# Performance work log

Measured on AMD Instinct MI355X. Metric: run time of the kernel, lower is better.

## Reference

```python
import jax, jax.numpy as jnp
import numpy as np

N_NODES = 100000
N_EDGES = 1600000
N_GRAPHS = 2048
BN_EPS = 1e-5


def _bn(h, gamma, beta):
    # BatchNorm1d in training mode: biased batch stats over the node axis
    mean = jnp.mean(h, axis=0)
    var = jnp.var(h, axis=0)
    return gamma * (h - mean) * jax.lax.rsqrt(var + BN_EPS) + beta


def _gin_layer(x, src, dst, w1, b1, gamma, beta, w2, b2):
    # GINConv with eps=0: mlp(x + sum_{j->i} x_j)
    agg = jax.ops.segment_sum(x[src], dst, num_segments=N_NODES)
    h = agg + x
    h = h @ w1 + b1
    h = jax.nn.relu(_bn(h, gamma, beta))
    h = h @ w2 + b2
    return jax.nn.relu(h)  # outer F.relu after GINConv (dropout = identity in eval)


def setup_inputs() -> dict:
    key = jax.random.key(0)
    ks = jax.random.split(key, 24)
    d = {}
    d['x'] = jax.random.normal(ks[0], (N_NODES, 66), dtype=jnp.float32)
    d['edge_index'] = jax.random.randint(ks[1], (2, N_EDGES), 0, N_NODES, dtype=jnp.int64)
    d['batch'] = jnp.sort(jax.random.randint(ks[2], (N_NODES,), 0, N_GRAPHS, dtype=jnp.int64))
    dims = [(66, 128), (128, 256), (256, 128)]
    ki = 3
    for li, (din, dout) in enumerate(dims):
        s1 = 1.0 / np.sqrt(din)
        s2 = 1.0 / np.sqrt(dout)
        d[f'g{li}_w1'] = jax.random.uniform(ks[ki + 0], (din, dout), jnp.float32, -s1, s1)
        d[f'g{li}_b1'] = jax.random.uniform(ks[ki + 1], (dout,), jnp.float32, -s1, s1)
        d[f'g{li}_gamma'] = jnp.ones((dout,), jnp.float32)
        d[f'g{li}_beta'] = jnp.zeros((dout,), jnp.float32)
        d[f'g{li}_w2'] = jax.random.uniform(ks[ki + 2], (dout, dout), jnp.float32, -s2, s2)
        d[f'g{li}_b2'] = jax.random.uniform(ks[ki + 3], (dout,), jnp.float32, -s2, s2)
        ki += 4
    fcd = [(128, 1024), (1024, 128)]
    for li, (din, dout) in enumerate(fcd):
        s = 1.0 / np.sqrt(din)
        d[f'fc{li}_w'] = jax.random.uniform(ks[ki + 0], (din, dout), jnp.float32, -s, s)
        d[f'fc{li}_b'] = jax.random.uniform(ks[ki + 1], (dout,), jnp.float32, -s, s)
        ki += 2
    return d


def reference(x, edge_index, batch,
              g0_w1, g0_b1, g0_gamma, g0_beta, g0_w2, g0_b2,
              g1_w1, g1_b1, g1_gamma, g1_beta, g1_w2, g1_b2,
              g2_w1, g2_b1, g2_gamma, g2_beta, g2_w2, g2_b2,
              fc0_w, fc0_b, fc1_w, fc1_b):
    src, dst = edge_index[0], edge_index[1]
    h = _gin_layer(x, src, dst, g0_w1, g0_b1, g0_gamma, g0_beta, g0_w2, g0_b2)
    h = _gin_layer(h, src, dst, g1_w1, g1_b1, g1_gamma, g1_beta, g1_w2, g1_b2)
    h = _gin_layer(h, src, dst, g2_w1, g2_b1, g2_gamma, g2_beta, g2_w2, g2_b2)
    # global_add_pool over graphs
    g = jax.ops.segment_sum(h, batch, num_segments=N_GRAPHS)
    g = jax.nn.relu(g @ fc0_w + fc0_b)
    return g @ fc1_w + fc1_b
```

## Files before the change

kernel.cpp:

```cpp
#include <hip/hip_runtime.h>

#define NNODES 100000
#define NEDGES 1600000
#define NGRAPHS 2048
#define BN_EPS 1e-5f

typedef __attribute__((ext_vector_type(8))) short bf16x8;
typedef __attribute__((ext_vector_type(4))) float f32x4;

__device__ __forceinline__ short f2bf(float x) {
    unsigned u = __float_as_uint(x);
    unsigned r = u + 0x7FFF + ((u >> 16) & 1);
    return (short)(r >> 16);
}
__device__ __forceinline__ float bf2f(short h) {
    return __uint_as_float(((unsigned)(unsigned short)h) << 16);
}

__global__ __launch_bounds__(256) void degoff_kernel(const int* __restrict__ dstA,
                                                     int* __restrict__ degp,
                                                     int* __restrict__ off) {
    int e = blockIdx.x * 256 + threadIdx.x;
    if (e < NEDGES) {
        int d = dstA[e];
        int c = atomicAdd(&degp[d << 4], 1);
        off[e] = (d << 8) | c;
    }
}

__global__ __launch_bounds__(256) void scan1_kernel(const int* __restrict__ degp,
                                                    int* __restrict__ partials) {
    int b = blockIdx.x;
    int i = b * 256 + threadIdx.x;
    int v = (i < NNODES) ? degp[i << 4] : 0;
    __shared__ int wsum[4];
#pragma unroll
    for (int off = 32; off; off >>= 1) v += __shfl_down(v, off);
    if ((threadIdx.x & 63) == 0) wsum[threadIdx.x >> 6] = v;
    __syncthreads();
    if (threadIdx.x == 0) partials[b] = wsum[0] + wsum[1] + wsum[2] + wsum[3];
}

__global__ __launch_bounds__(512) void scan2_kernel(int* __restrict__ partials, int nb) {
    __shared__ int s[512];
    int t = threadIdx.x;
    int v = (t < nb) ? partials[t] : 0;
    s[t] = v;
    __syncthreads();
    for (int off = 1; off < 512; off <<= 1) {
        int u = (t >= off) ? s[t - off] : 0;
        __syncthreads();
        s[t] += u;
        __syncthreads();
    }
    if (t < nb) partials[t] = s[t] - v;
}

__global__ __launch_bounds__(256) void scan3_kernel(const int* __restrict__ degp,
                                                    const int* __restrict__ partials,
                                                    int* __restrict__ rowptr,
                                                    const int* __restrict__ batch,
                                                    int* __restrict__ gstart) {
    int b = blockIdx.x;
    int t = threadIdx.x;
    int i = b * 256 + t;
    __shared__ int s[256];
    int v = (i < NNODES) ? degp[i << 4] : 0;
    s[t] = v;
    __syncthreads();
    for (int off = 1; off < 256; off <<= 1) {
        int u = (t >= off) ? s[t - off] : 0;
        __syncthreads();
        s[t] += u;
        __syncthreads();
    }
    if (i < NNODES) {
        int ex = partials[b] + s[t] - v;
        rowptr[i] = ex;
        int bb = batch[i];
        int bp = (i == 0) ? -1 : batch[i - 1];
        for (int g = bp + 1; g <= bb; ++g) gstart[g] = i;
        if (i == NNODES - 1)
            for (int g = bb + 1; g <= NGRAPHS; ++g) gstart[g] = NNODES;
    }
    if (b == 0 && t == 0) rowptr[NNODES] = NEDGES;
}

__global__ __launch_bounds__(256) void fill2_kernel(const int* __restrict__ srcA,
                                                    const int* __restrict__ rowptr,
                                                    const int* __restrict__ off,
                                                    int* __restrict__ adj) {
    int e = blockIdx.x * 256 + threadIdx.x;
    if (e < NEDGES) {
        int v = off[e];
        adj[rowptr[v >> 8] + (v & 255)] = srcA[e];
    }
}

__global__ __launch_bounds__(256) void pad66_kernel(const float* __restrict__ x,
                                                    float* __restrict__ xpad) {
    int idx = blockIdx.x * 256 + threadIdx.x;
    if (idx >= NNODES * 17) return;
    int node = idx / 17;
    int c = idx - node * 17;
    float4 v;
    if (c < 16) {
        float2 a = *(const float2*)&x[(size_t)node * 66 + c * 4];
        float2 b = *(const float2*)&x[(size_t)node * 66 + c * 4 + 2];
        v = make_float4(a.x, a.y, b.x, b.y);
    } else {
        float2 a = *(const float2*)&x[(size_t)node * 66 + 64];
        v = make_float4(a.x, a.y, 0.f, 0.f);
    }
    *(float4*)&xpad[(size_t)node * 68 + c * 4] = v;
}

template <int DIM, int CHUNK, int OSTRIDE, bool SPLIT>
__global__ __launch_bounds__(256) void gather_kernel(const float* __restrict__ x,
                                                     const int* __restrict__ rowptr,
                                                     const int* __restrict__ adj,
                                                     float* __restrict__ agg,
                                                     short* __restrict__ oh,
                                                     short* __restrict__ ol,
                                                     const float* __restrict__ bias) {
    constexpr int PE = DIM / CHUNK;
    constexpr int PEL = SPLIT ? (OSTRIDE / CHUNK) : PE;
    int gid = blockIdx.x * 256 + threadIdx.x;
    if (gid >= NNODES * PEL) return;
    int node = gid / PEL;
    int c = gid - node * PEL;
    if constexpr (SPLIT) {
        if (c >= PE) {
            size_t o = (size_t)node * OSTRIDE + c * CHUNK;
            if constexpr (CHUNK == 4) {
                short4 z;
                z.x = z.y = z.z = z.w = 0;
                *(short4*)&oh[o] = z;
                *(short4*)&ol[o] = z;
            } else {
                short2 z;
                z.x = z.y = 0;
                *(short2*)&oh[o] = z;
                *(short2*)&ol[o] = z;
            }
            return;
        }
    }
    const int beg = rowptr[node];
    const int end = rowptr[node + 1];
    if constexpr (CHUNK == 4) {
        const float4* xp = (const float4*)x;
        float4 acc = xp[(size_t)node * PE + c];
        float4 acc1 = make_float4(0.f, 0.f, 0.f, 0.f);
        int i = beg;
        for (; i + 8 <= end; i += 8) {
            int s0 = adj[i + 0], s1 = adj[i + 1], s2 = adj[i + 2], s3 = adj[i + 3];
            int s4 = adj[i + 4], s5 = adj[i + 5], s6 = adj[i + 6], s7 = adj[i + 7];
            float4 v0 = xp[(size_t)s0 * PE + c];
            float4 v1 = xp[(size_t)s1 * PE + c];
            float4 v2 = xp[(size_t)s2 * PE + c];
            float4 v3 = xp[(size_t)s3 * PE + c];
            float4 v4 = xp[(size_t)s4 * PE + c];
            float4 v5 = xp[(size_t)s5 * PE + c];
            float4 v6 = xp[(size_t)s6 * PE + c];
            float4 v7 = xp[(size_t)s7 * PE + c];
            acc.x += v0.x + v1.x; acc.y += v0.y + v1.y; acc.z += v0.z + v1.z; acc.w += v0.w + v1.w;
            acc1.x += v2.x + v3.x; acc1.y += v2.y + v3.y; acc1.z += v2.z + v3.z; acc1.w += v2.w + v3.w;
            acc.x += v4.x + v5.x; acc.y += v4.y + v5.y; acc.z += v4.z + v5.z; acc.w += v4.w + v5.w;
            acc1.x += v6.x + v7.x; acc1.y += v6.y + v7.y; acc1.z += v6.z + v7.z; acc1.w += v6.w + v7.w;
        }
        for (; i + 4 <= end; i += 4) {
            int s0 = adj[i + 0], s1 = adj[i + 1], s2 = adj[i + 2], s3 = adj[i + 3];
            float4 v0 = xp[(size_t)s0 * PE + c];
            float4 v1 = xp[(size_t)s1 * PE + c];
            float4 v2 = xp[(size_t)s2 * PE + c];
            float4 v3 = xp[(size_t)s3 * PE + c];
            acc.x += v0.x + v1.x; acc.y += v0.y + v1.y; acc.z += v0.z + v1.z; acc.w += v0.w + v1.w;
            acc1.x += v2.x + v3.x; acc1.y += v2.y + v3.y; acc1.z += v2.z + v3.z; acc1.w += v2.w + v3.w;
        }
        for (; i < end; ++i) {
            int s = adj[i];
            float4 v = xp[(size_t)s * PE + c];
            acc.x += v.x; acc.y += v.y; acc.z += v.z; acc.w += v.w;
        }
        acc.x += acc1.x; acc.y += acc1.y; acc.z += acc1.z; acc.w += acc1.w;
        if (bias) {
            float4 b = *(const float4*)&bias[c * 4];
            acc.x += b.x; acc.y += b.y; acc.z += b.z; acc.w += b.w;
        }
        if constexpr (SPLIT) {
            size_t o = (size_t)node * OSTRIDE + c * 4;
            short4 h4, l4;
            h4.x = f2bf(acc.x); l4.x = f2bf(acc.x - bf2f(h4.x));
            h4.y = f2bf(acc.y); l4.y = f2bf(acc.y - bf2f(h4.y));
            h4.z = f2bf(acc.z); l4.z = f2bf(acc.z - bf2f(h4.z));
            h4.w = f2bf(acc.w); l4.w = f2bf(acc.w - bf2f(h4.w));
            *(short4*)&oh[o] = h4;
            *(short4*)&ol[o] = l4;
        } else {
            *(float4*)&agg[(size_t)node * OSTRIDE + c * 4] = acc;
        }
    } else {
        const float2* xp = (const float2*)x;
        float2 acc = xp[(size_t)node * PE + c];
        float2 acc1 = make_float2(0.f, 0.f);
        int i = beg;
        for (; i + 8 <= end; i += 8) {
            int s0 = adj[i + 0], s1 = adj[i + 1], s2 = adj[i + 2], s3 = adj[i + 3];
            int s4 = adj[i + 4], s5 = adj[i + 5], s6 = adj[i + 6], s7 = adj[i + 7];
            float2 v0 = xp[(size_t)s0 * PE + c];
            float2 v1 = xp[(size_t)s1 * PE + c];
            float2 v2 = xp[(size_t)s2 * PE + c];
            float2 v3 = xp[(size_t)s3 * PE + c];
            float2 v4 = xp[(size_t)s4 * PE + c];
            float2 v5 = xp[(size_t)s5 * PE + c];
            float2 v6 = xp[(size_t)s6 * PE + c];
            float2 v7 = xp[(size_t)s7 * PE + c];
            acc.x += v0.x + v1.x; acc.y += v0.y + v1.y;
            acc1.x += v2.x + v3.x; acc1.y += v2.y + v3.y;
            acc.x += v4.x + v5.x; acc.y += v4.y + v5.y;
            acc1.x += v6.x + v7.x; acc1.y += v6.y + v7.y;
        }
        for (; i + 4 <= end; i += 4) {
            int s0 = adj[i + 0], s1 = adj[i + 1], s2 = adj[i + 2], s3 = adj[i + 3];
            float2 v0 = xp[(size_t)s0 * PE + c];
            float2 v1 = xp[(size_t)s1 * PE + c];
            float2 v2 = xp[(size_t)s2 * PE + c];
            float2 v3 = xp[(size_t)s3 * PE + c];
            acc.x += v0.x + v1.x; acc.y += v0.y + v1.y;
            acc1.x += v2.x + v3.x; acc1.y += v2.y + v3.y;
        }
        for (; i < end; ++i) {
            int s = adj[i];
            float2 v = xp[(size_t)s * PE + c];
            acc.x += v.x; acc.y += v.y;
        }
        acc.x += acc1.x; acc.y += acc1.y;
        if constexpr (SPLIT) {
            size_t o = (size_t)node * OSTRIDE + c * 2;
            short2 h2, l2;
            h2.x = f2bf(acc.x); l2.x = f2bf(acc.x - bf2f(h2.x));
            h2.y = f2bf(acc.y); l2.y = f2bf(acc.y - bf2f(h2.y));
            *(short2*)&oh[o] = h2;
            *(short2*)&ol[o] = l2;
        } else {
            *(float2*)&agg[(size_t)node * OSTRIDE + c * 2] = acc;
        }
    }
}

template <int N>
__global__ __launch_bounds__(256) void bnstats_kernel(const float* __restrict__ h,
                                                      float* __restrict__ sums) {
    constexpr int SHIFT = (N == 128) ? 7 : 8;
    int t = blockIdx.x * 256 + threadIdx.x;
    int col = t & (N - 1);
    int slice = t >> SHIFT;
    int stride = (gridDim.x * 256) >> SHIFT;
    float s = 0.f, s2 = 0.f;
    for (int r = slice; r < NNODES; r += stride) {
        float v = h[(size_t)r * N + col];
        s += v;
        s2 += v * v;
    }
    atomicAdd(&sums[col], s);
    atomicAdd(&sums[256 + col], s2);
}

__global__ void bnfinal_kernel(float* __restrict__ sums, const float* __restrict__ gamma,
                               const float* __restrict__ beta, float* __restrict__ scsh, int N,
                               float invM) {
    int c = threadIdx.x;
    if (c < N) {
        float mean = sums[c] * invM;
        float var = sums[256 + c] * invM - mean * mean;
        float sc = gamma[c] * rsqrtf(var + BN_EPS);
        scsh[c] = sc;
        scsh[256 + c] = beta[c] - mean * sc;
    }
    sums[c] = 0.f;
    sums[256 + c] = 0.f;
}

struct WDesc {
    const float* W;
    int Kw, N, KT, hioff, looff;
};
struct WDescs {
    WDesc d[8];
    int cum[9];
};
__global__ __launch_bounds__(256) void wprep_all_kernel(WDescs wd, short* __restrict__ wf) {
    int idx = blockIdx.x * 256 + threadIdx.x;
    if (idx >= wd.cum[8]) return;
    int s = 0;
#pragma unroll
    for (int i = 1; i < 8; ++i) s += (idx >= wd.cum[i]);
    int r = idx - wd.cum[s];
    const WDesc D = wd.d[s];
    int j = r & 7;
    int lane = (r >> 3) & 63;
    int t = r >> 9;
    int kt = t % D.KT;
    int nt = t / D.KT;
    int k = kt * 32 + ((lane >> 4) << 3) + j;
    int n = (nt << 4) + (lane & 15);
    float w = (k < D.Kw) ? D.W[(size_t)k * D.N + n] : 0.f;
    short hi = f2bf(w);
    wf[D.hioff + r] = hi;
    wf[D.looff + r] = f2bf(w - bf2f(hi));
}

template <int NT, int KTLOOP, int KTT, int MROWS, bool BNRELU_A, bool RELU_OUT, bool FUSE_STATS,
          bool SPLITK, bool ASPLIT, bool SPLIT_OUT, int MINW>
__global__ __launch_bounds__(256, MINW) void gemm_mfma_kernel(
    const float* __restrict__ A, const short* __restrict__ Ah, const short* __restrict__ Al,
    const short* __restrict__ whi, const short* __restrict__ wlo, const float* __restrict__ bias,
    const float* __restrict__ scsh, float* __restrict__ C, short* __restrict__ Ch,
    short* __restrict__ Cl, float* __restrict__ stats, int M, int Kst, int N) {
    __shared__ float sstat[512];
    const int tid = threadIdx.x;
    const int wave = tid >> 6;
    const int lane = tid & 63;
    const int quad = lane >> 4;
    const int l16 = lane & 15;
    const int mrow = blockIdx.x * (64 * MROWS) + wave * 16 + l16;
    const int ngrp = blockIdx.y * NT * 16;
    const size_t wgrp = (size_t)blockIdx.y * NT * KTT * 512;
    const int ktbeg = SPLITK ? blockIdx.z * KTLOOP : 0;
    float* Cb = SPLITK ? C + (size_t)blockIdx.z * M * N : C;

    if (FUSE_STATS) {
        sstat[tid] = 0.f;
        sstat[tid + 256] = 0.f;
        __syncthreads();
    }

    f32x4 acc[MROWS][NT] = {};

    auto kstep = [&](int kt) {
        const int kq = kt * 32 + quad * 8;
        bf16x8 ahi[MROWS], alo[MROWS];
        if constexpr (ASPLIT) {
#pragma unroll
            for (int m = 0; m < MROWS; ++m) {
                const size_t ro = (size_t)(mrow + m * 64) * Kst + kq;
                ahi[m] = *(const bf16x8*)(Ah + ro);
                alo[m] = *(const bf16x8*)(Al + ro);
            }
        } else {
            float sc[8], sh[8];
            if constexpr (BNRELU_A) {
                float4 sc0 = *(const float4*)&scsh[kq];
                float4 sc1 = *(const float4*)&scsh[kq + 4];
                float4 sh0 = *(const float4*)&scsh[256 + kq];
                float4 sh1 = *(const float4*)&scsh[256 + kq + 4];
                sc[0] = sc0.x; sc[1] = sc0.y; sc[2] = sc0.z; sc[3] = sc0.w;
                sc[4] = sc1.x; sc[5] = sc1.y; sc[6] = sc1.z; sc[7] = sc1.w;
                sh[0] = sh0.x; sh[1] = sh0.y; sh[2] = sh0.z; sh[3] = sh0.w;
                sh[4] = sh1.x; sh[5] = sh1.y; sh[6] = sh1.z; sh[7] = sh1.w;
            }
#pragma unroll
            for (int m = 0; m < MROWS; ++m) {
                const float* ap = A + (size_t)(mrow + m * 64) * Kst + kq;
                float4 x0 = *(const float4*)ap;
                float4 x1 = *(const float4*)(ap + 4);
                float a8[8] = {x0.x, x0.y, x0.z, x0.w, x1.x, x1.y, x1.z, x1.w};
                if constexpr (BNRELU_A) {
#pragma unroll
                    for (int i = 0; i < 8; ++i) a8[i] = fmaxf(a8[i] * sc[i] + sh[i], 0.f);
                }
#pragma unroll
                for (int i = 0; i < 8; ++i) {
                    short h = f2bf(a8[i]);
                    ahi[m][i] = h;
                    alo[m][i] = f2bf(a8[i] - bf2f(h));
                }
            }
        }
#pragma unroll
        for (int nt = 0; nt < NT; ++nt) {
            const size_t boff = wgrp + (((size_t)nt * KTT + kt) << 9) + ((size_t)lane << 3);
            bf16x8 bh = *(const bf16x8*)(whi + boff);
            bf16x8 bl = *(const bf16x8*)(wlo + boff);
#pragma unroll
            for (int m = 0; m < MROWS; ++m) {
                acc[m][nt] = __builtin_amdgcn_mfma_f32_16x16x32_bf16(ahi[m], bh, acc[m][nt], 0, 0, 0);
                acc[m][nt] = __builtin_amdgcn_mfma_f32_16x16x32_bf16(alo[m], bh, acc[m][nt], 0, 0, 0);
                acc[m][nt] = __builtin_amdgcn_mfma_f32_16x16x32_bf16(ahi[m], bl, acc[m][nt], 0, 0, 0);
                acc[m][nt] = __builtin_amdgcn_mfma_f32_16x16x32_bf16(alo[m], bl, acc[m][nt], 0, 0, 0);
            }
        }
    };

    if constexpr (ASPLIT) {
#pragma unroll 2
        for (int k = 0; k < KTLOOP; ++k) kstep(ktbeg + k);
    } else {
#pragma unroll 1
        for (int k = 0; k < KTLOOP; ++k) kstep(ktbeg + k);
    }

#pragma unroll
    for (int m = 0; m < MROWS; ++m) {
        const int mbase = blockIdx.x * (64 * MROWS) + m * 64 + wave * 16 + quad * 4;
#pragma unroll
        for (int nt = 0; nt < NT; ++nt) {
            int gn = ngrp + nt * 16 + l16;
            float bv = bias ? bias[gn] : 0.f;
            float s = 0.f, s2 = 0.f;
#pragma unroll
            for (int r = 0; r < 4; ++r) {
                int gm = mbase + r;
                float v = acc[m][nt][r] + bv;
                if (RELU_OUT) v = fmaxf(v, 0.f);
                if (gm < M) {
                    if constexpr (SPLIT_OUT) {
                        short h = f2bf(v);
                        Ch[(size_t)gm * N + gn] = h;
                        Cl[(size_t)gm * N + gn] = f2bf(v - bf2f(h));
                    } else {
                        Cb[(size_t)gm * N + gn] = v;
                    }
                    if (FUSE_STATS) {
                        s += v;
                        s2 += v * v;
                    }
                }
            }
            if (FUSE_STATS) {
                s += __shfl_xor(s, 16);
                s += __shfl_xor(s, 32);
                s2 += __shfl_xor(s2, 16);
                s2 += __shfl_xor(s2, 32);
                if (quad == 0) {
                    atomicAdd(&sstat[gn], s);
                    atomicAdd(&sstat[256 + gn], s2);
                }
            }
        }
    }
    if (FUSE_STATS) {
        __syncthreads();
        if (tid < N) {
            atomicAdd(&stats[tid], sstat[tid]);
            atomicAdd(&stats[256 + tid], sstat[256 + tid]);
        }
    }
}

__global__ __launch_bounds__(256) void splitk_reduce_kernel(const float* __restrict__ part,
                                                            const float* __restrict__ bias,
                                                            float* __restrict__ out) {
    const int i4 = blockIdx.x * 256 + threadIdx.x;
    const int TOT4 = NGRAPHS * 128 / 4;
    if (i4 >= TOT4) return;
    const float4* p = (const float4*)part;
    float4 acc = make_float4(0.f, 0.f, 0.f, 0.f);
#pragma unroll
    for (int c = 0; c < 8; ++c) {
        float4 v = p[(size_t)c * TOT4 + i4];
        acc.x += v.x;
        acc.y += v.y;
        acc.z += v.z;
        acc.w += v.w;
    }
    float4 b = ((const float4*)bias)[i4 & 31];
    acc.x += b.x;
    acc.y += b.y;
    acc.z += b.z;
    acc.w += b.w;
    ((float4*)out)[i4] = acc;
}

template <bool SPLIT>
__global__ __launch_bounds__(128) void pool_seg_kernel(const float* __restrict__ h,
                                                       const int* __restrict__ gstart,
                                                       float* __restrict__ g,
                                                       short* __restrict__ oh,
                                                       short* __restrict__ ol) {
    int gr = blockIdx.x;
    int t = threadIdx.x;
    int beg = gstart[gr];
    int end = gstart[gr + 1];
    float acc = 0.f;
    for (int r = beg; r < end; ++r) acc += h[(size_t)r * 128 + t];
    if constexpr (SPLIT) {
        short hh = f2bf(acc);
        oh[(size_t)gr * 128 + t] = hh;
        ol[(size_t)gr * 128 + t] = f2bf(acc - bf2f(hh));
    } else {
        g[(size_t)gr * 128 + t] = acc;
    }
}

extern "C" void kernel_launch(void* const* d_in, const int* in_sizes, int n_in, void* d_out,
                              int out_size, void* d_ws, size_t ws_size, hipStream_t stream) {
    const float* x = (const float*)d_in[0];
    const int* ei = (const int*)d_in[1];
    const int* batch = (const int*)d_in[2];
    const int* srcA = ei;
    const int* dstA = ei + NEDGES;

    const float* g0_w1 = (const float*)d_in[3];
    const float* g0_b1 = (const float*)d_in[4];
    const float* g0_ga = (const float*)d_in[5];
    const float* g0_be = (const float*)d_in[6];
    const float* g0_w2 = (const float*)d_in[7];
    const float* g0_b2 = (const float*)d_in[8];
    const float* g1_w1 = (const float*)d_in[9];
    const float* g1_b1 = (const float*)d_in[10];
    const float* g1_ga = (const float*)d_in[11];
    const float* g1_be = (const float*)d_in[12];
    const float* g1_w2 = (const float*)d_in[13];
    const float* g1_b2 = (const float*)d_in[14];
    const float* g2_w1 = (const float*)d_in[15];
    const float* g2_b1 = (const float*)d_in[16];
    const float* g2_ga = (const float*)d_in[17];
    const float* g2_be = (const float*)d_in[18];
    const float* g2_w2 = (const float*)d_in[19];
    const float* g2_b2 = (const float*)d_in[20];
    const float* fc0_w = (const float*)d_in[21];
    const float* fc0_b = (const float*)d_in[22];
    const float* fc1_w = (const float*)d_in[23];
    const float* fc1_b = (const float*)d_in[24];

    float* ws = (float*)d_ws;
    const size_t BUF = (size_t)NNODES * 256;
    float* R0 = ws;
    float* R1 = R0 + BUF;
    float* stats = R1 + BUF;
    float* scsh = stats + 512;
    float* g = scsh + 512;
    float* gh = g + (size_t)NGRAPHS * 128;
    int* rowptr = (int*)(gh + (size_t)NGRAPHS * 1024);
    int* adj = rowptr + NNODES + 4;
    int* partials = adj + NEDGES;
    int* gstart = partials + 512;
    short* wf = (short*)(gstart + 2052);

    int* degp = (int*)R0;
    int* off = degp + NNODES * 16;
    float* xpad = R1;

    short* whi[8];
    short* wlo[8];
    for (int i = 0; i < 6; ++i) {
        whi[i] = wf + (size_t)i * 131072;
        wlo[i] = whi[i] + 65536;
    }
    whi[6] = wf + 6 * 131072;
    wlo[6] = whi[6] + 131072;
    whi[7] = whi[6] + 262144;
    wlo[7] = whi[7] + 131072;

    short* P0h = (short*)R0;
    short* P0l = P0h + (size_t)NNODES * 96;
    short* P1h = (short*)R1;
    short* P1l = P1h + (size_t)NNODES * 128;
    short* P2h = (short*)R1;
    short* P2l = P2h + (size_t)NNODES * 256;
    short* GPh = (short*)g;
    short* GPl = GPh + (size_t)NGRAPHS * 128;
    short* GHh = (short*)gh;
    short* GHl = GHh + (size_t)NGRAPHS * 1024;

    const int GB2 = (NNODES + 127) / 128;
    const int GB3 = (NNODES + 191) / 192;
    const int NB = (NNODES + 255) / 256;
    const int EB = (NEDGES + 255) / 256;

    hipMemsetAsync(degp, 0, (size_t)NNODES * 16 * sizeof(int), stream);
    hipMemsetAsync(stats, 0, 512 * sizeof(float), stream);
    pad66_kernel<<<(NNODES * 17 + 255) / 256, 256, 0, stream>>>(x, xpad);
    degoff_kernel<<<EB, 256, 0, stream>>>(dstA, degp, off);
    scan1_kernel<<<NB, 256, 0, stream>>>(degp, partials);
    scan2_kernel<<<1, 512, 0, stream>>>(partials, NB);
    scan3_kernel<<<NB, 256, 0, stream>>>(degp, partials, rowptr, batch, gstart);
    fill2_kernel<<<EB, 256, 0, stream>>>(srcA, rowptr, off, adj);

    {
        WDescs wd;
        const float* Wp[8] = {g0_w1, g0_w2, g1_w1, g1_w2, g2_w1, g2_w2, fc0_w, fc1_w};
        const int Kw[8] = {66, 128, 128, 256, 256, 128, 128, 1024};
        const int Nn[8] = {128, 128, 256, 256, 128, 128, 1024, 128};
        const int KT[8] = {3, 4, 4, 8, 8, 4, 4, 32};
        int cum = 0;
        wd.cum[0] = 0;
        for (int i = 0; i < 8; ++i) {
            wd.d[i].W = Wp[i];
            wd.d[i].Kw = Kw[i];
            wd.d[i].N = Nn[i];
            wd.d[i].KT = KT[i];
            wd.d[i].hioff = (int)(whi[i] - wf);
            wd.d[i].looff = (int)(wlo[i] - wf);
            cum += (Nn[i] >> 4) * KT[i] * 512;
            wd.cum[i + 1] = cum;
        }
        wprep_all_kernel<<<(wd.cum[8] + 255) / 256, 256, 0, stream>>>(wd, wf);
    }

    gather_kernel<68, 4, 96, true><<<(NNODES * 24 + 255) / 256, 256, 0, stream>>>(
        xpad, rowptr, adj, nullptr, P0h, P0l, nullptr);
    gemm_mfma_kernel<8, 3, 3, 3, false, false, true, false, true, false, 2>
        <<<GB3, 256, 0, stream>>>(nullptr, P0h, P0l, whi[0], wlo[0], g0_b1, nullptr, R1, nullptr,
                                  nullptr, stats, NNODES, 96, 128);
    bnfinal_kernel<<<1, 256, 0, stream>>>(stats, g0_ga, g0_be, scsh, 128, 1.0f / NNODES);
    gemm_mfma_kernel<8, 4, 4, 2, true, true, false, false, false, false, 3>
        <<<GB2, 256, 0, stream>>>(R1, nullptr, nullptr, whi[1], wlo[1], g0_b2, scsh, R0, nullptr,
                                  nullptr, nullptr, NNODES, 128, 128);

    gather_kernel<128, 4, 128, true><<<(NNODES * 32 + 255) / 256, 256, 0, stream>>>(
        R0, rowptr, adj, nullptr, P1h, P1l, nullptr);
    gemm_mfma_kernel<8, 4, 4, 3, false, false, true, false, true, false, 2>
        <<<dim3(GB3, 2), 256, 0, stream>>>(nullptr, P1h, P1l, whi[2], wlo[2], g1_b1, nullptr, R0,
                                           nullptr, nullptr, stats, NNODES, 128, 256);
    bnfinal_kernel<<<1, 256, 0, stream>>>(stats, g1_ga, g1_be, scsh, 256, 1.0f / NNODES);
    gemm_mfma_kernel<8, 8, 8, 2, true, true, false, false, false, true, 3>
        <<<dim3(GB2, 2), 256, 0, stream>>>(R0, nullptr, nullptr, whi[3], wlo[3], g1_b2, scsh,
                                           nullptr, P2h, P2l, nullptr, NNODES, 256, 256);

    gemm_mfma_kernel<8, 8, 8, 3, false, false, false, false, true, false, 2>
        <<<GB3, 256, 0, stream>>>(nullptr, P2h, P2l, whi[4], wlo[4], nullptr, nullptr, R0, nullptr,
                                  nullptr, nullptr, NNODES, 256, 128);
    gather_kernel<128, 4, 128, false><<<(NNODES * 32 + 255) / 256, 256, 0, stream>>>(
        R0, rowptr, adj, R1, nullptr, nullptr, g2_b1);
    bnstats_kernel<128><<<256, 256, 0, stream>>>(R1, stats);
    bnfinal_kernel<<<1, 256, 0, stream>>>(stats, g2_ga, g2_be, scsh, 128, 1.0f / NNODES);
    gemm_mfma_kernel<8, 4, 4, 2, true, true, false, false, false, false, 3>
        <<<GB2, 256, 0, stream>>>(R1, nullptr, nullptr, whi[5], wlo[5], g2_b2, scsh, R0, nullptr,
                                  nullptr, nullptr, NNODES, 128, 128);

    pool_seg_kernel<true><<<NGRAPHS, 128, 0, stream>>>(R0, gstart, nullptr, GPh, GPl);

    gemm_mfma_kernel<8, 4, 4, 2, false, true, false, false, true, true, 3>
        <<<dim3(NGRAPHS / 128, 8), 256, 0, stream>>>(nullptr, GPh, GPl, whi[6], wlo[6], fc0_b,
                                                     nullptr, nullptr, GHh, GHl, nullptr, NGRAPHS,
                                                     128, 1024);
    gemm_mfma_kernel<8, 4, 32, 2, false, false, false, true, true, false, 3>
        <<<dim3(NGRAPHS / 128, 1, 8), 256, 0, stream>>>(nullptr, GHh, GHl, whi[7], wlo[7], nullptr,
                                                        nullptr, R1, nullptr, nullptr, nullptr,
                                                        NGRAPHS, 1024, 128);
    splitk_reduce_kernel<<<(NGRAPHS * 128 / 4 + 255) / 256, 256, 0, stream>>>(R1, fc1_b,
                                                                              (float*)d_out);
}
```

Measured before the change: 1.134 ms.

## Fold BatchNorm finalize into consuming GEMM prologue and drop MROWS=3 tiles

Removes the three single-block bnfinal launches. Each BN-consuming GEMM block now computes scale and shift from the raw stats, gamma and beta into shared memory in its prologue, and each layer gets its own stats buffer so no reset is needed. The GEMMs that used 3 row tiles per wave with occupancy hint 2 are switched to 2 row tiles with hint 3. This saves launch gaps and trades per-block redundant finalize work and a barrier for fewer serialized kernels, while the tiling change alters reuse and occupancy.

```diff
diff --git a/kernel.cpp b/kernel.cpp
--- a/kernel.cpp
+++ b/kernel.cpp
@@ -267,21 +267,6 @@
     atomicAdd(&sums[256 + col], s2);
 }
 
-__global__ void bnfinal_kernel(float* __restrict__ sums, const float* __restrict__ gamma,
-                               const float* __restrict__ beta, float* __restrict__ scsh, int N,
-                               float invM) {
-    int c = threadIdx.x;
-    if (c < N) {
-        float mean = sums[c] * invM;
-        float var = sums[256 + c] * invM - mean * mean;
-        float sc = gamma[c] * rsqrtf(var + BN_EPS);
-        scsh[c] = sc;
-        scsh[256 + c] = beta[c] - mean * sc;
-    }
-    sums[c] = 0.f;
-    sums[256 + c] = 0.f;
-}
-
 struct WDesc {
     const float* W;
     int Kw, N, KT, hioff, looff;
@@ -316,9 +301,11 @@
 __global__ __launch_bounds__(256, MINW) void gemm_mfma_kernel(
     const float* __restrict__ A, const short* __restrict__ Ah, const short* __restrict__ Al,
     const short* __restrict__ whi, const short* __restrict__ wlo, const float* __restrict__ bias,
-    const float* __restrict__ scsh, float* __restrict__ C, short* __restrict__ Ch,
-    short* __restrict__ Cl, float* __restrict__ stats, int M, int Kst, int N) {
-    __shared__ float sstat[512];
+    const float* __restrict__ gamma, const float* __restrict__ beta, float* __restrict__ C,
+    short* __restrict__ Ch, short* __restrict__ Cl, float* __restrict__ stats, int M, int Kst,
+    int N) {
+    static_assert(!(FUSE_STATS && BNRELU_A), "sbuf is shared between the two roles");
+    __shared__ float sbuf[512];
     const int tid = threadIdx.x;
     const int wave = tid >> 6;
     const int lane = tid & 63;
@@ -331,8 +318,19 @@
     float* Cb = SPLITK ? C + (size_t)blockIdx.z * M * N : C;
 
     if (FUSE_STATS) {
-        sstat[tid] = 0.f;
-        sstat[tid + 256] = 0.f;
+        sbuf[tid] = 0.f;
+        sbuf[tid + 256] = 0.f;
+        __syncthreads();
+    }
+    if (BNRELU_A) {
+        if (tid < Kst) {
+            const float invM = 1.0f / NNODES;
+            float mean = stats[tid] * invM;
+            float var = stats[256 + tid] * invM - mean * mean;
+            float sc = gamma[tid] * rsqrtf(var + BN_EPS);
+            sbuf[tid] = sc;
+            sbuf[256 + tid] = beta[tid] - mean * sc;
+        }
         __syncthreads();
     }
 
@@ -351,10 +349,10 @@
         } else {
             float sc[8], sh[8];
             if constexpr (BNRELU_A) {
-                float4 sc0 = *(const float4*)&scsh[kq];
-                float4 sc1 = *(const float4*)&scsh[kq + 4];
-                float4 sh0 = *(const float4*)&scsh[256 + kq];
-                float4 sh1 = *(const float4*)&scsh[256 + kq + 4];
+                float4 sc0 = *(const float4*)&sbuf[kq];
+                float4 sc1 = *(const float4*)&sbuf[kq + 4];
+                float4 sh0 = *(const float4*)&sbuf[256 + kq];
+                float4 sh1 = *(const float4*)&sbuf[256 + kq + 4];
                 sc[0] = sc0.x; sc[1] = sc0.y; sc[2] = sc0.z; sc[3] = sc0.w;
                 sc[4] = sc1.x; sc[5] = sc1.y; sc[6] = sc1.z; sc[7] = sc1.w;
                 sh[0] = sh0.x; sh[1] = sh0.y; sh[2] = sh0.z; sh[3] = sh0.w;
@@ -434,8 +432,8 @@
                 s2 += __shfl_xor(s2, 16);
                 s2 += __shfl_xor(s2, 32);
                 if (quad == 0) {
-                    atomicAdd(&sstat[gn], s);
-                    atomicAdd(&sstat[256 + gn], s2);
+                    atomicAdd(&sbuf[gn], s);
+                    atomicAdd(&sbuf[256 + gn], s2);
                 }
             }
         }
@@ -443,8 +441,8 @@
     if (FUSE_STATS) {
         __syncthreads();
         if (tid < N) {
-            atomicAdd(&stats[tid], sstat[tid]);
-            atomicAdd(&stats[256 + tid], sstat[256 + tid]);
+            atomicAdd(&stats[tid], sbuf[tid]);
+            atomicAdd(&stats[256 + tid], sbuf[256 + tid]);
         }
     }
 }
@@ -529,9 +527,10 @@
     const size_t BUF = (size_t)NNODES * 256;
     float* R0 = ws;
     float* R1 = R0 + BUF;
-    float* stats = R1 + BUF;
-    float* scsh = stats + 512;
-    float* g = scsh + 512;
+    float* stats0 = R1 + BUF;
+    float* stats1 = stats0 + 512;
+    float* stats2 = stats1 + 512;
+    float* g = stats2 + 512;
     float* gh = g + (size_t)NGRAPHS * 128;
     int* rowptr = (int*)(gh + (size_t)NGRAPHS * 1024);
     int* adj = rowptr + NNODES + 4;
@@ -566,12 +565,11 @@
     short* GHl = GHh + (size_t)NGRAPHS * 1024;
 
     const int GB2 = (NNODES + 127) / 128;
-    const int GB3 = (NNODES + 191) / 192;
     const int NB = (NNODES + 255) / 256;
     const int EB = (NEDGES + 255) / 256;
 
     hipMemsetAsync(degp, 0, (size_t)NNODES * 16 * sizeof(int), stream);
-    hipMemsetAsync(stats, 0, 512 * sizeof(float), stream);
+    hipMemsetAsync(stats0, 0, 1536 * sizeof(float), stream);
     pad66_kernel<<<(NNODES * 17 + 255) / 256, 256, 0, stream>>>(x, xpad);
     degoff_kernel<<<EB, 256, 0, stream>>>(dstA, degp, off);
     scan1_kernel<<<NB, 256, 0, stream>>>(degp, partials);
@@ -602,45 +600,43 @@
 
     gather_kernel<68, 4, 96, true><<<(NNODES * 24 + 255) / 256, 256, 0, stream>>>(
         xpad, rowptr, adj, nullptr, P0h, P0l, nullptr);
-    gemm_mfma_kernel<8, 3, 3, 3, false, false, true, false, true, false, 2>
-        <<<GB3, 256, 0, stream>>>(nullptr, P0h, P0l, whi[0], wlo[0], g0_b1, nullptr, R1, nullptr,
-                                  nullptr, stats, NNODES, 96, 128);
-    bnfinal_kernel<<<1, 256, 0, stream>>>(stats, g0_ga, g0_be, scsh, 128, 1.0f / NNODES);
+    gemm_mfma_kernel<8, 3, 3, 2, false, false, true, false, true, false, 3>
+        <<<GB2, 256, 0, stream>>>(nullptr, P0h, P0l, whi[0], wlo[0], g0_b1, nullptr, nullptr, R1,
+                                  nullptr, nullptr, stats0, NNODES, 96, 128);
     gemm_mfma_kernel<8, 4, 4, 2, true, true, false, false, false, false, 3>
-        <<<GB2, 256, 0, stream>>>(R1, nullptr, nullptr, whi[1], wlo[1], g0_b2, scsh, R0, nullptr,
-                                  nullptr, nullptr, NNODES, 128, 128);
+        <<<GB2, 256, 0, stream>>>(R1, nullptr, nullptr, whi[1], wlo[1], g0_b2, g0_ga, g0_be, R0,
+                                  nullptr, nullptr, stats0, NNODES, 128, 128);
 
     gather_kernel<128, 4, 128, true><<<(NNODES * 32 + 255) / 256, 256, 0, stream>>>(
         R0, rowptr, adj, nullptr, P1h, P1l, nullptr);
-    gemm_mfma_kernel<8, 4, 4, 3, false, false, true, false, true, false, 2>
-        <<<dim3(GB3, 2), 256, 0, stream>>>(nullptr, P1h, P1l, whi[2], wlo[2], g1_b1, nullptr, R0,
-                                           nullptr, nullptr, stats, NNODES, 128, 256);
-    bnfinal_kernel<<<1, 256, 0, stream>>>(stats, g1_ga, g1_be, scsh, 256, 1.0f / NNODES);
+    gemm_mfma_kernel<8, 4, 4, 2, false, false, true, false, true, false, 3>
+        <<<dim3(GB2, 2), 256, 0, stream>>>(nullptr, P1h, P1l, whi[2], wlo[2], g1_b1, nullptr,
+                                           nullptr, R0, nullptr, nullptr, stats1, NNODES, 128,
+                                           256);
     gemm_mfma_kernel<8, 8, 8, 2, true, true, false, false, false, true, 3>
-        <<<dim3(GB2, 2), 256, 0, stream>>>(R0, nullptr, nullptr, whi[3], wlo[3], g1_b2, scsh,
-                                           nullptr, P2h, P2l, nullptr, NNODES, 256, 256);
-
-    gemm_mfma_kernel<8, 8, 8, 3, false, false, false, false, true, false, 2>
-        <<<GB3, 256, 0, stream>>>(nullptr, P2h, P2l, whi[4], wlo[4], nullptr, nullptr, R0, nullptr,
-                                  nullptr, nullptr, NNODES, 256, 128);
+        <<<dim3(GB2, 2), 256, 0, stream>>>(R0, nullptr, nullptr, whi[3], wlo[3], g1_b2, g1_ga,
+                                           g1_be, nullptr, P2h, P2l, stats1, NNODES, 256, 256);
+
+    gemm_mfma_kernel<8, 8, 8, 2, false, false, false, false, true, false, 3>
+        <<<GB2, 256, 0, stream>>>(nullptr, P2h, P2l, whi[4], wlo[4], nullptr, nullptr, nullptr,
+                                  R0, nullptr, nullptr, nullptr, NNODES, 256, 128);
     gather_kernel<128, 4, 128, false><<<(NNODES * 32 + 255) / 256, 256, 0, stream>>>(
         R0, rowptr, adj, R1, nullptr, nullptr, g2_b1);
-    bnstats_kernel<128><<<256, 256, 0, stream>>>(R1, stats);
-    bnfinal_kernel<<<1, 256, 0, stream>>>(stats, g2_ga, g2_be, scsh, 128, 1.0f / NNODES);
+    bnstats_kernel<128><<<256, 256, 0, stream>>>(R1, stats2);
     gemm_mfma_kernel<8, 4, 4, 2, true, true, false, false, false, false, 3>
-        <<<GB2, 256, 0, stream>>>(R1, nullptr, nullptr, whi[5], wlo[5], g2_b2, scsh, R0, nullptr,
-                                  nullptr, nullptr, NNODES, 128, 128);
+        <<<GB2, 256, 0, stream>>>(R1, nullptr, nullptr, whi[5], wlo[5], g2_b2, g2_ga, g2_be, R0,
+                                  nullptr, nullptr, stats2, NNODES, 128, 128);
 
     pool_seg_kernel<true><<<NGRAPHS, 128, 0, stream>>>(R0, gstart, nullptr, GPh, GPl);
 
     gemm_mfma_kernel<8, 4, 4, 2, false, true, false, false, true, true, 3>
         <<<dim3(NGRAPHS / 128, 8), 256, 0, stream>>>(nullptr, GPh, GPl, whi[6], wlo[6], fc0_b,
-                                                     nullptr, nullptr, GHh, GHl, nullptr, NGRAPHS,
-                                                     128, 1024);
+                                                     nullptr, nullptr, nullptr, GHh, GHl, nullptr,
+                                                     NGRAPHS, 128, 1024);
     gemm_mfma_kernel<8, 4, 32, 2, false, false, false, true, true, false, 3>
         <<<dim3(NGRAPHS / 128, 1, 8), 256, 0, stream>>>(nullptr, GHh, GHl, whi[7], wlo[7], nullptr,
-                                                        nullptr, R1, nullptr, nullptr, nullptr,
-                                                        NGRAPHS, 1024, 128);
+                                                        nullptr, nullptr, R1, nullptr, nullptr,
+                                                        nullptr, NGRAPHS, 1024, 128);
     splitk_reduce_kernel<<<(NGRAPHS * 128 / 4 + 255) / 256, 256, 0, stream>>>(R1, fc1_b,
                                                                               (float*)d_out);
 }
```

Result: slower. 1.162 ms (+2.5%).
